# Optimization experiments

Hardware: AMD Instinct MI355X
Metric: run time of the kernel (lower is better)

## Reference

```python
import jax, jax.numpy as jnp
import numpy as np
import math

B, S, D = 2, 4096, 512
H, DK, DV = 8, 64, 64

def setup_inputs() -> dict:
    key = jax.random.key(0)
    ks = jax.random.split(key, 11)
    sc = lambda fin: 1.0 / math.sqrt(fin)
    return {
        "q": jax.random.normal(ks[0], (B, S, D), jnp.float32),
        "k": jax.random.normal(ks[1], (B, S, D), jnp.float32),
        "v": jax.random.normal(ks[2], (B, S, D), jnp.float32),
        "Wq": jax.random.normal(ks[3], (D, H * DK), jnp.float32) * sc(D),
        "bq": jnp.zeros((H * DK,), jnp.float32),
        "Wk": jax.random.normal(ks[4], (D, H * DK), jnp.float32) * sc(D),
        "bk": jnp.zeros((H * DK,), jnp.float32),
        "Wv": jax.random.normal(ks[5], (D, H * DV), jnp.float32) * sc(D),
        "bv": jnp.zeros((H * DV,), jnp.float32),
        "Wo": jax.random.normal(ks[6], (H * DV, D), jnp.float32) * sc(H * DV),
        "bo": jnp.zeros((D,), jnp.float32),
    }

def reference(q, k, v, Wq, bq, Wk, bk, Wv, bv, Wo, bo):
    b = q.shape[0]
    # projections -> [b, h, s, d]
    qh = (q @ Wq + bq).reshape(b, -1, H, DK).transpose(0, 2, 1, 3)
    kh = (k @ Wk + bk).reshape(b, -1, H, DK).transpose(0, 2, 1, 3)
    vh = (v @ Wv + bv).reshape(b, -1, H, DV).transpose(0, 2, 1, 3)
    # scores: [b, h, sq, sk]
    scores = jnp.einsum("bhqd,bhkd->bhqk", qh, kh) / math.sqrt(DK)
    # NOTE: faithful to source, softmax over dim=-2 (the QUERY axis)
    attn = jax.nn.softmax(scores, axis=-2)
    out = jnp.einsum("bhqk,bhkd->bhqd", attn, vh)
    out = out.transpose(0, 2, 1, 3).reshape(b, -1, H * DV)
    return out @ Wo + bo
```

## Files before the change

kernel.cpp:

```cpp
#include <hip/hip_runtime.h>
#include <math.h>

namespace {

typedef short bf8_t __attribute__((ext_vector_type(8)));
typedef float f32x4 __attribute__((ext_vector_type(4)));
typedef unsigned short u16;

constexpr int kB = 2, kS = 4096, kD = 512, kH = 8, kBH = 16;
constexpr float kScale = 0.125f;

__device__ __forceinline__ u16 f2bf(float x) {
  const unsigned u = __float_as_uint(x);
  return (u16)((u + 0x7FFFu + ((u >> 16) & 1u)) >> 16);
}
__device__ __forceinline__ float bf2f(u16 h) {
  return __uint_as_float(((unsigned)h) << 16);
}

template <int MODE>
__global__ __launch_bounds__(256) void gemm_kernel(
    const float* __restrict__ A, const float* __restrict__ W,
    const float* __restrict__ bias, u16* __restrict__ oHi,
    u16* __restrict__ oLo, float* __restrict__ oF) {
  __shared__ float As[16][68];
  __shared__ float Ws[16][68];
  const int t = threadIdx.x;
  const int m0 = blockIdx.y * 64;
  const int n0 = blockIdx.x * 64;
  const int ty = t >> 4, tx = t & 15;
  const int lam = t >> 2, lac = t & 3;
  const int lwk = t >> 4, lwn = t & 15;

  float acc[4][4] = {};

  for (int k0 = 0; k0 < kD; k0 += 16) {
    const float4 av = *(const float4*)&A[(size_t)(m0 + lam) * kD + k0 + lac * 4];
    const float4 wv = *(const float4*)&W[(size_t)(k0 + lwk) * kD + n0 + lwn * 4];
    __syncthreads();
    As[lac * 4 + 0][lam] = av.x;
    As[lac * 4 + 1][lam] = av.y;
    As[lac * 4 + 2][lam] = av.z;
    As[lac * 4 + 3][lam] = av.w;
    *(float4*)&Ws[lwk][lwn * 4] = wv;
    __syncthreads();
#pragma unroll
    for (int kk = 0; kk < 16; ++kk) {
      const float4 a4 = *(const float4*)&As[kk][ty * 4];
      const float4 b4 = *(const float4*)&Ws[kk][tx * 4];
      const float a[4] = {a4.x, a4.y, a4.z, a4.w};
      const float b[4] = {b4.x, b4.y, b4.z, b4.w};
#pragma unroll
      for (int i = 0; i < 4; ++i)
#pragma unroll
        for (int j = 0; j < 4; ++j) acc[i][j] = fmaf(a[i], b[j], acc[i][j]);
    }
  }

  float bb[4];
#pragma unroll
  for (int j = 0; j < 4; ++j) bb[j] = bias[n0 + tx * 4 + j];

  if (MODE == 0) {
    const int h = n0 >> 6;
#pragma unroll
    for (int i = 0; i < 4; ++i) {
      const int m = m0 + ty * 4 + i;
      const int bI = m >> 12, s = m & (kS - 1);
      const int bh = bI * kH + h;
      union { u16 u[4]; uint2 q; } ph, pl;
#pragma unroll
      for (int j = 0; j < 4; ++j) {
        const float x = acc[i][j] + bb[j];
        ph.u[j] = f2bf(x);
        pl.u[j] = f2bf(x - bf2f(ph.u[j]));
      }
      const size_t off = ((size_t)bh * kS + s) * 64 + tx * 4;
      *(uint2*)&oHi[off] = ph.q;
      *(uint2*)&oLo[off] = pl.q;
    }
  } else if (MODE == 2) {
    const int h = n0 >> 6;
    const int bI = m0 >> 12;
    const int s0 = (m0 & (kS - 1)) + ty * 4;
    const int bh = bI * kH + h;
#pragma unroll
    for (int j = 0; j < 4; ++j) {
      const int dv = tx * 4 + j;
      float4 ov;
      ov.x = acc[0][j] + bb[j];
      ov.y = acc[1][j] + bb[j];
      ov.z = acc[2][j] + bb[j];
      ov.w = acc[3][j] + bb[j];
      *(float4*)&oF[((size_t)(bh * 64 + dv)) * kS + s0] = ov;
    }
  } else {
#pragma unroll
    for (int i = 0; i < 4; ++i) {
      const int m = m0 + ty * 4 + i;
      float4 ov;
      ov.x = acc[i][0] + bb[0];
      ov.y = acc[i][1] + bb[1];
      ov.z = acc[i][2] + bb[2];
      ov.w = acc[i][3] + bb[3];
      *(float4*)&oF[(size_t)m * kD + n0 + tx * 4] = ov;
    }
  }
}

__global__ __launch_bounds__(256) void colstats_kernel(
    const u16* __restrict__ Qhi, const u16* __restrict__ Qlo,
    const u16* __restrict__ Khi, const u16* __restrict__ Klo,
    float* __restrict__ Rl) {
  const int nid = (int)blockIdx.x;
  const int swz = (nid & 7) * 128 + (nid >> 3);
  const int bh = swz >> 6;
  const int k0 = (swz & 63) << 6;
  const int t = threadIdx.x;
  const int w = t >> 6, l = t & 63;
  const int lr = l & 15, lg = l >> 4;
  const size_t base = (size_t)bh * kS * 64;

  bf8_t kbh[4][2], kbl[4][2];
#pragma unroll
  for (int nt = 0; nt < 4; ++nt)
#pragma unroll
    for (int kh = 0; kh < 2; ++kh) {
      const size_t off = base + (size_t)(k0 + nt * 16 + lr) * 64 + kh * 32 + lg * 8;
      kbh[nt][kh] = *(const bf8_t*)&Khi[off];
      kbl[nt][kh] = *(const bf8_t*)&Klo[off];
    }

  float lsum[4] = {0.f, 0.f, 0.f, 0.f};

  for (int q0 = 0; q0 < kS; q0 += 64) {
    bf8_t qah[2], qal[2];
    const size_t qoff = base + (size_t)(q0 + w * 16 + lr) * 64;
#pragma unroll
    for (int kh = 0; kh < 2; ++kh) {
      qah[kh] = *(const bf8_t*)&Qhi[qoff + kh * 32 + lg * 8];
      qal[kh] = *(const bf8_t*)&Qlo[qoff + kh * 32 + lg * 8];
    }
#pragma unroll
    for (int nt = 0; nt < 4; ++nt) {
      f32x4 acc = {0.f, 0.f, 0.f, 0.f};
#pragma unroll
      for (int kh = 0; kh < 2; ++kh) {
        acc = __builtin_amdgcn_mfma_f32_16x16x32_bf16(qah[kh], kbh[nt][kh], acc, 0, 0, 0);
        acc = __builtin_amdgcn_mfma_f32_16x16x32_bf16(qah[kh], kbl[nt][kh], acc, 0, 0, 0);
        acc = __builtin_amdgcn_mfma_f32_16x16x32_bf16(qal[kh], kbh[nt][kh], acc, 0, 0, 0);
      }
#pragma unroll
      for (int r = 0; r < 4; ++r) lsum[nt] += __expf(acc[r] * kScale);
    }
  }

#pragma unroll
  for (int nt = 0; nt < 4; ++nt) {
    float s = lsum[nt];
    s += __shfl_xor(s, 16, 64);
    s += __shfl_xor(s, 32, 64);
    lsum[nt] = s;
  }
  __shared__ float red[4][64];
  if (l < 16) {
#pragma unroll
    for (int nt = 0; nt < 4; ++nt) red[w][nt * 16 + l] = lsum[nt];
  }
  __syncthreads();
  if (t < 64) {
    const float s = red[0][t] + red[1][t] + red[2][t] + red[3][t];
    Rl[(size_t)bh * kS + k0 + t] = 1.0f / s;
  }
}

__global__ __launch_bounds__(256) void scale_split_kernel(
    const float* __restrict__ Vf, const float* __restrict__ Rl,
    u16* __restrict__ Vsh, u16* __restrict__ Vsl) {
  const int idx = blockIdx.x * 256 + threadIdx.x;
  const int s4 = (idx & 1023) << 2;
  const int bhdv = idx >> 10;
  const int bh = bhdv >> 6;
  const float4 v = *(const float4*)&Vf[(size_t)bhdv * kS + s4];
  const float4 r = *(const float4*)&Rl[(size_t)bh * kS + s4];
  const float x[4] = {v.x * r.x, v.y * r.y, v.z * r.z, v.w * r.w};
  union { u16 u[4]; uint2 q; } hh, ll;
#pragma unroll
  for (int j = 0; j < 4; ++j) {
    hh.u[j] = f2bf(x[j]);
    ll.u[j] = f2bf(x[j] - bf2f(hh.u[j]));
  }
  *(uint2*)&Vsh[(size_t)bhdv * kS + s4] = hh.q;
  *(uint2*)&Vsl[(size_t)bhdv * kS + s4] = ll.q;
}

__global__ __launch_bounds__(256) void attn_kernel(
    const u16* __restrict__ Qhi, const u16* __restrict__ Qlo,
    const u16* __restrict__ Khi, const u16* __restrict__ Klo,
    const u16* __restrict__ Vsh, const u16* __restrict__ Vsl,
    float* __restrict__ AttnOut) {
  __shared__ u16 KsH[64 * 72], KsL[64 * 72];
  __shared__ u16 VpH[64 * 72], VpL[64 * 72];

  const int nid = (int)blockIdx.x;
  const int swz = (nid & 7) * 64 + (nid >> 3);
  const int bh = swz >> 5;
  const int q0 = (swz & 31) << 7;
  const int t = threadIdx.x;
  const int w = t >> 6, l = t & 63;
  const int lr = l & 15, lg = l >> 4;
  const size_t base = (size_t)bh * kS * 64;

  const int srow = t >> 3;
  const int sc = t & 7;
  const int sc8 = sc * 8;
  const int sub = sc & 3, half = sub >> 1;
  const int posA = ((sc >> 2) << 5) + ((sub & 1) << 4) + (half << 2);

  bf8_t qh[2][2], ql[2][2];
#pragma unroll
  for (int nt = 0; nt < 2; ++nt) {
    const size_t qoff = base + (size_t)(q0 + w * 32 + nt * 16 + lr) * 64;
#pragma unroll
    for (int kh = 0; kh < 2; ++kh) {
      qh[nt][kh] = *(const bf8_t*)&Qhi[qoff + kh * 32 + lg * 8];
      ql[nt][kh] = *(const bf8_t*)&Qlo[qoff + kh * 32 + lg * 8];
    }
  }

  f32x4 acco[4][2];
  {
    const f32x4 z = {0.f, 0.f, 0.f, 0.f};
#pragma unroll
    for (int mt = 0; mt < 4; ++mt)
#pragma unroll
      for (int nt = 0; nt < 2; ++nt) acco[mt][nt] = z;
  }

  uint4 rkh[2], rkl[2], rvh[2], rvl[2];
#pragma unroll
  for (int ri = 0; ri < 2; ++ri) {
    const int row = srow + ri * 32;
    rkh[ri] = *(const uint4*)&Khi[base + (size_t)row * 64 + sc8];
    rkl[ri] = *(const uint4*)&Klo[base + (size_t)row * 64 + sc8];
    rvh[ri] = *(const uint4*)&Vsh[(size_t)(bh * 64 + row) * kS + sc8];
    rvl[ri] = *(const uint4*)&Vsl[(size_t)(bh * 64 + row) * kS + sc8];
  }

  for (int kt = 0; kt < kS / 64; ++kt) {
    __syncthreads();
#pragma unroll
    for (int ri = 0; ri < 2; ++ri) {
      const int row = srow + ri * 32;
      *(uint4*)&KsH[row * 72 + sc8] = rkh[ri];
      *(uint4*)&KsL[row * 72 + sc8] = rkl[ri];
      uint2 a, b;
      a.x = rvh[ri].x; a.y = rvh[ri].y; b.x = rvh[ri].z; b.y = rvh[ri].w;
      *(uint2*)&VpH[row * 72 + posA] = a;
      *(uint2*)&VpH[row * 72 + posA + 8] = b;
      a.x = rvl[ri].x; a.y = rvl[ri].y; b.x = rvl[ri].z; b.y = rvl[ri].w;
      *(uint2*)&VpL[row * 72 + posA] = a;
      *(uint2*)&VpL[row * 72 + posA + 8] = b;
    }
    __syncthreads();

    if (kt + 1 < kS / 64) {
      const int k0n = (kt + 1) * 64;
#pragma unroll
      for (int ri = 0; ri < 2; ++ri) {
        const int row = srow + ri * 32;
        rkh[ri] = *(const uint4*)&Khi[base + (size_t)(k0n + row) * 64 + sc8];
        rkl[ri] = *(const uint4*)&Klo[base + (size_t)(k0n + row) * 64 + sc8];
        rvh[ri] = *(const uint4*)&Vsh[(size_t)(bh * 64 + row) * kS + k0n + sc8];
        rvl[ri] = *(const uint4*)&Vsl[(size_t)(bh * 64 + row) * kS + k0n + sc8];
      }
    }

    f32x4 accs[4][2];
#pragma unroll
    for (int mt = 0; mt < 4; ++mt) {
      bf8_t kfh[2], kfl[2];
#pragma unroll
      for (int kh = 0; kh < 2; ++kh) {
        kfh[kh] = *(const bf8_t*)&KsH[(mt * 16 + lr) * 72 + kh * 32 + lg * 8];
        kfl[kh] = *(const bf8_t*)&KsL[(mt * 16 + lr) * 72 + kh * 32 + lg * 8];
      }
#pragma unroll
      for (int nt = 0; nt < 2; ++nt) {
        f32x4 a = {0.f, 0.f, 0.f, 0.f};
#pragma unroll
        for (int kh = 0; kh < 2; ++kh) {
          a = __builtin_amdgcn_mfma_f32_16x16x32_bf16(kfh[kh], qh[nt][kh], a, 0, 0, 0);
          a = __builtin_amdgcn_mfma_f32_16x16x32_bf16(kfh[kh], ql[nt][kh], a, 0, 0, 0);
          a = __builtin_amdgcn_mfma_f32_16x16x32_bf16(kfl[kh], qh[nt][kh], a, 0, 0, 0);
        }
        accs[mt][nt] = a;
      }
    }

    bf8_t ph[2][2], pl[2][2];
#pragma unroll
    for (int nt = 0; nt < 2; ++nt)
#pragma unroll
      for (int kh = 0; kh < 2; ++kh) {
        union { u16 u[8]; bf8_t v; } uh, ul;
#pragma unroll
        for (int r = 0; r < 4; ++r) {
          const float x0 = __expf(accs[2 * kh][nt][r] * kScale);
          const u16 h0 = f2bf(x0);
          uh.u[r] = h0;
          ul.u[r] = f2bf(x0 - bf2f(h0));
          const float x1 = __expf(accs[2 * kh + 1][nt][r] * kScale);
          const u16 h1 = f2bf(x1);
          uh.u[4 + r] = h1;
          ul.u[4 + r] = f2bf(x1 - bf2f(h1));
        }
        ph[nt][kh] = uh.v;
        pl[nt][kh] = ul.v;
      }

#pragma unroll
    for (int mt = 0; mt < 4; ++mt) {
      bf8_t vfh[2], vfl[2];
#pragma unroll
      for (int kh = 0; kh < 2; ++kh) {
        vfh[kh] = *(const bf8_t*)&VpH[(mt * 16 + lr) * 72 + kh * 32 + lg * 8];
        vfl[kh] = *(const bf8_t*)&VpL[(mt * 16 + lr) * 72 + kh * 32 + lg * 8];
      }
#pragma unroll
      for (int nt = 0; nt < 2; ++nt) {
        f32x4 a = acco[mt][nt];
#pragma unroll
        for (int kh = 0; kh < 2; ++kh) {
          a = __builtin_amdgcn_mfma_f32_16x16x32_bf16(vfh[kh], ph[nt][kh], a, 0, 0, 0);
          a = __builtin_amdgcn_mfma_f32_16x16x32_bf16(vfh[kh], pl[nt][kh], a, 0, 0, 0);
          a = __builtin_amdgcn_mfma_f32_16x16x32_bf16(vfl[kh], ph[nt][kh], a, 0, 0, 0);
        }
        acco[mt][nt] = a;
      }
    }
  }

  const int bI = bh >> 3, h = bh & 7;
#pragma unroll
  for (int mt = 0; mt < 4; ++mt)
#pragma unroll
    for (int nt = 0; nt < 2; ++nt) {
      const int q = q0 + w * 32 + nt * 16 + lr;
#pragma unroll
      for (int r = 0; r < 4; ++r) {
        const int dv = mt * 16 + lg * 4 + r;
        AttnOut[((size_t)(bI * kS + q)) * kD + h * 64 + dv] = acco[mt][nt][r];
      }
    }
}

}

extern "C" void kernel_launch(void* const* d_in, const int* in_sizes, int n_in,
                              void* d_out, int out_size, void* d_ws,
                              size_t ws_size, hipStream_t stream) {
  (void)in_sizes; (void)n_in; (void)out_size; (void)ws_size;
  const float* q  = (const float*)d_in[0];
  const float* k  = (const float*)d_in[1];
  const float* v  = (const float*)d_in[2];
  const float* Wq = (const float*)d_in[3];
  const float* bq = (const float*)d_in[4];
  const float* Wk = (const float*)d_in[5];
  const float* bk = (const float*)d_in[6];
  const float* Wv = (const float*)d_in[7];
  const float* bv = (const float*)d_in[8];
  const float* Wo = (const float*)d_in[9];
  const float* bo = (const float*)d_in[10];
  float* out = (float*)d_out;

  const size_t hE = (size_t)kBH * kS * 64;
  u16* Qhi = (u16*)d_ws;
  u16* Qlo = Qhi + hE;
  u16* Khi = Qlo + hE;
  u16* Klo = Khi + hE;
  u16* Vsh = Klo + hE;
  u16* Vsl = Vsh + hE;
  float* Vf = (float*)(Vsl + hE);
  float* Rl = Vf + hE;
  float* AttnOut = Vf;

  const dim3 gemmGrid(kD / 64, (kB * kS) / 64);

  gemm_kernel<0><<<gemmGrid, 256, 0, stream>>>(q, Wq, bq, Qhi, Qlo, nullptr);
  gemm_kernel<0><<<gemmGrid, 256, 0, stream>>>(k, Wk, bk, Khi, Klo, nullptr);
  gemm_kernel<2><<<gemmGrid, 256, 0, stream>>>(v, Wv, bv, nullptr, nullptr, Vf);
  colstats_kernel<<<1024, 256, 0, stream>>>(Qhi, Qlo, Khi, Klo, Rl);
  scale_split_kernel<<<4096, 256, 0, stream>>>(Vf, Rl, Vsh, Vsl);
  attn_kernel<<<512, 256, 0, stream>>>(Qhi, Qlo, Khi, Klo, Vsh, Vsl, AttnOut);
  gemm_kernel<1><<<gemmGrid, 256, 0, stream>>>(AttnOut, Wo, bo, nullptr, nullptr, out);
}
```

Measured before the change: 704.7 us.

## Move projection GEMMs to split-bf16 MFMA and swizzle LDS layouts

The FP32 FMA projection GEMMs are replaced with MFMA-based GEMMs using a hi/lo bf16 split (three MFMAs per tile), with new kernels that pre-split inputs and pre-transpose and split the weights. Other changes ride along: colstats stages Q tiles through swizzled LDS with register prefetch, attention uses XOR-swizzled LDS instead of padding, the attention output is written pre-split through an LDS transpose, and V transposition plus scaling moves into a tiled kernel. Rounding in the split now truncates the hi part instead of rounding to nearest, which could change accuracy. Extra launches and workspace traffic are added for splitting the inputs and weights.

```diff
diff --git a/kernel.cpp b/kernel.cpp
--- a/kernel.cpp
+++ b/kernel.cpp
@@ -10,100 +10,185 @@
 constexpr int kB = 2, kS = 4096, kD = 512, kH = 8, kBH = 16;
 constexpr float kScale = 0.125f;
 
-__device__ __forceinline__ u16 f2bf(float x) {
+__device__ __forceinline__ void split2(float x, u16& hi, u16& lo) {
   const unsigned u = __float_as_uint(x);
-  return (u16)((u + 0x7FFFu + ((u >> 16) & 1u)) >> 16);
-}
-__device__ __forceinline__ float bf2f(u16 h) {
-  return __uint_as_float(((unsigned)h) << 16);
+  hi = (u16)(u >> 16);
+  const float r = x - __uint_as_float(u & 0xFFFF0000u);
+  lo = (u16)(__float_as_uint(r) >> 16);
+}
+
+__global__ __launch_bounds__(256) void split_kernel(
+    const float* __restrict__ src, u16* __restrict__ dhi,
+    u16* __restrict__ dlo) {
+  const size_t i4 = ((size_t)blockIdx.x * 256 + threadIdx.x) * 4;
+  const float4 v = *(const float4*)&src[i4];
+  union { u16 u[4]; uint2 q; } h, l;
+  split2(v.x, h.u[0], l.u[0]);
+  split2(v.y, h.u[1], l.u[1]);
+  split2(v.z, h.u[2], l.u[2]);
+  split2(v.w, h.u[3], l.u[3]);
+  *(uint2*)&dhi[i4] = h.q;
+  *(uint2*)&dlo[i4] = l.q;
+}
+
+__global__ __launch_bounds__(256) void splitT_kernel(
+    const float* __restrict__ W, u16* __restrict__ whi,
+    u16* __restrict__ wlo) {
+  __shared__ float Ls[64][68];
+  const int t = threadIdx.x;
+  const int n0 = blockIdx.x * 64, k0 = blockIdx.y * 64;
+#pragma unroll
+  for (int i = 0; i < 4; ++i) {
+    const int kl = (t >> 4) + i * 16;
+    const int n4 = (t & 15) * 4;
+    const float4 v = *(const float4*)&W[(size_t)(k0 + kl) * kD + n0 + n4];
+    Ls[kl][n4 + 0] = v.x; Ls[kl][n4 + 1] = v.y;
+    Ls[kl][n4 + 2] = v.z; Ls[kl][n4 + 3] = v.w;
+  }
+  __syncthreads();
+#pragma unroll
+  for (int i = 0; i < 4; ++i) {
+    const int nl = (t >> 4) + i * 16;
+    const int k4 = (t & 15) * 4;
+    union { u16 u[4]; uint2 q; } h, l;
+#pragma unroll
+    for (int j = 0; j < 4; ++j) split2(Ls[k4 + j][nl], h.u[j], l.u[j]);
+    *(uint2*)&whi[(size_t)(n0 + nl) * kD + k0 + k4] = h.q;
+    *(uint2*)&wlo[(size_t)(n0 + nl) * kD + k0 + k4] = l.q;
+  }
 }
 
 template <int MODE>
-__global__ __launch_bounds__(256) void gemm_kernel(
-    const float* __restrict__ A, const float* __restrict__ W,
+__global__ __launch_bounds__(256) void mfma_gemm_kernel(
+    const u16* __restrict__ Ahi, const u16* __restrict__ Alo,
+    const u16* __restrict__ Whi, const u16* __restrict__ Wlo,
     const float* __restrict__ bias, u16* __restrict__ oHi,
     u16* __restrict__ oLo, float* __restrict__ oF) {
-  __shared__ float As[16][68];
-  __shared__ float Ws[16][68];
+  __shared__ u16 gsm[24576];
+  u16* AhS = gsm;
+  u16* AlS = gsm + 8192;
+  u16* WhS = gsm + 16384;
+  u16* WlS = gsm + 20480;
+
   const int t = threadIdx.x;
-  const int m0 = blockIdx.y * 64;
+  const int w = t >> 6, l = t & 63;
+  const int lr = l & 15, lg = l >> 4;
+  const int m0 = blockIdx.y * 128;
   const int n0 = blockIdx.x * 64;
-  const int ty = t >> 4, tx = t & 15;
-  const int lam = t >> 2, lac = t & 3;
-  const int lwk = t >> 4, lwn = t & 15;
-
-  float acc[4][4] = {};
-
-  for (int k0 = 0; k0 < kD; k0 += 16) {
-    const float4 av = *(const float4*)&A[(size_t)(m0 + lam) * kD + k0 + lac * 4];
-    const float4 wv = *(const float4*)&W[(size_t)(k0 + lwk) * kD + n0 + lwn * 4];
+
+  f32x4 acc[2][4];
+  {
+    const f32x4 z = {0.f, 0.f, 0.f, 0.f};
+#pragma unroll
+    for (int mt = 0; mt < 2; ++mt)
+#pragma unroll
+      for (int nt = 0; nt < 4; ++nt) acc[mt][nt] = z;
+  }
+
+  uint4 rAh[4], rAl[4], rWh[2], rWl[2];
+#pragma unroll
+  for (int i = 0; i < 4; ++i) {
+    const int p = t + i * 256, row = p >> 3, c = p & 7;
+    rAh[i] = *(const uint4*)&Ahi[(size_t)(m0 + row) * kD + c * 8];
+    rAl[i] = *(const uint4*)&Alo[(size_t)(m0 + row) * kD + c * 8];
+  }
+#pragma unroll
+  for (int i = 0; i < 2; ++i) {
+    const int p = t + i * 256, row = p >> 3, c = p & 7;
+    rWh[i] = *(const uint4*)&Whi[(size_t)(n0 + row) * kD + c * 8];
+    rWl[i] = *(const uint4*)&Wlo[(size_t)(n0 + row) * kD + c * 8];
+  }
+
+  for (int ks = 0; ks < 8; ++ks) {
     __syncthreads();
-    As[lac * 4 + 0][lam] = av.x;
-    As[lac * 4 + 1][lam] = av.y;
-    As[lac * 4 + 2][lam] = av.z;
-    As[lac * 4 + 3][lam] = av.w;
-    *(float4*)&Ws[lwk][lwn * 4] = wv;
+#pragma unroll
+    for (int i = 0; i < 4; ++i) {
+      const int p = t + i * 256, row = p >> 3, c = p & 7;
+      const int ch = (row * 8 + (c ^ (row & 7))) * 8;
+      *(uint4*)&AhS[ch] = rAh[i];
+      *(uint4*)&AlS[ch] = rAl[i];
+    }
+#pragma unroll
+    for (int i = 0; i < 2; ++i) {
+      const int p = t + i * 256, row = p >> 3, c = p & 7;
+      const int ch = (row * 8 + (c ^ (row & 7))) * 8;
+      *(uint4*)&WhS[ch] = rWh[i];
+      *(uint4*)&WlS[ch] = rWl[i];
+    }
     __syncthreads();
-#pragma unroll
-    for (int kk = 0; kk < 16; ++kk) {
-      const float4 a4 = *(const float4*)&As[kk][ty * 4];
-      const float4 b4 = *(const float4*)&Ws[kk][tx * 4];
-      const float a[4] = {a4.x, a4.y, a4.z, a4.w};
-      const float b[4] = {b4.x, b4.y, b4.z, b4.w};
-#pragma unroll
-      for (int i = 0; i < 4; ++i)
-#pragma unroll
-        for (int j = 0; j < 4; ++j) acc[i][j] = fmaf(a[i], b[j], acc[i][j]);
-    }
-  }
-
-  float bb[4];
-#pragma unroll
-  for (int j = 0; j < 4; ++j) bb[j] = bias[n0 + tx * 4 + j];
-
-  if (MODE == 0) {
-    const int h = n0 >> 6;
-#pragma unroll
-    for (int i = 0; i < 4; ++i) {
-      const int m = m0 + ty * 4 + i;
-      const int bI = m >> 12, s = m & (kS - 1);
-      const int bh = bI * kH + h;
-      union { u16 u[4]; uint2 q; } ph, pl;
-#pragma unroll
-      for (int j = 0; j < 4; ++j) {
-        const float x = acc[i][j] + bb[j];
-        ph.u[j] = f2bf(x);
-        pl.u[j] = f2bf(x - bf2f(ph.u[j]));
-      }
-      const size_t off = ((size_t)bh * kS + s) * 64 + tx * 4;
-      *(uint2*)&oHi[off] = ph.q;
-      *(uint2*)&oLo[off] = pl.q;
-    }
-  } else if (MODE == 2) {
-    const int h = n0 >> 6;
-    const int bI = m0 >> 12;
-    const int s0 = (m0 & (kS - 1)) + ty * 4;
-    const int bh = bI * kH + h;
-#pragma unroll
-    for (int j = 0; j < 4; ++j) {
-      const int dv = tx * 4 + j;
-      float4 ov;
-      ov.x = acc[0][j] + bb[j];
-      ov.y = acc[1][j] + bb[j];
-      ov.z = acc[2][j] + bb[j];
-      ov.w = acc[3][j] + bb[j];
-      *(float4*)&oF[((size_t)(bh * 64 + dv)) * kS + s0] = ov;
-    }
-  } else {
-#pragma unroll
-    for (int i = 0; i < 4; ++i) {
-      const int m = m0 + ty * 4 + i;
-      float4 ov;
-      ov.x = acc[i][0] + bb[0];
-      ov.y = acc[i][1] + bb[1];
-      ov.z = acc[i][2] + bb[2];
-      ov.w = acc[i][3] + bb[3];
-      *(float4*)&oF[(size_t)m * kD + n0 + tx * 4] = ov;
+
+    if (ks + 1 < 8) {
+      const int kk = (ks + 1) * 64;
+#pragma unroll
+      for (int i = 0; i < 4; ++i) {
+        const int p = t + i * 256, row = p >> 3, c = p & 7;
+        rAh[i] = *(const uint4*)&Ahi[(size_t)(m0 + row) * kD + kk + c * 8];
+        rAl[i] = *(const uint4*)&Alo[(size_t)(m0 + row) * kD + kk + c * 8];
+      }
+#pragma unroll
+      for (int i = 0; i < 2; ++i) {
+        const int p = t + i * 256, row = p >> 3, c = p & 7;
+        rWh[i] = *(const uint4*)&Whi[(size_t)(n0 + row) * kD + kk + c * 8];
+        rWl[i] = *(const uint4*)&Wlo[(size_t)(n0 + row) * kD + kk + c * 8];
+      }
+    }
+
+#pragma unroll
+    for (int kh = 0; kh < 2; ++kh) {
+#pragma unroll
+      for (int mt = 0; mt < 2; ++mt) {
+        const int ar = w * 32 + mt * 16 + lr;
+        const int au = (ar * 64 + ((kh * 32 + lg * 8) ^ ((ar & 7) * 8)));
+        const bf8_t ah = *(const bf8_t*)&AhS[au];
+        const bf8_t al = *(const bf8_t*)&AlS[au];
+#pragma unroll
+        for (int nt = 0; nt < 4; ++nt) {
+          const int br = nt * 16 + lr;
+          const int bu = (br * 64 + ((kh * 32 + lg * 8) ^ ((br & 7) * 8)));
+          const bf8_t bh = *(const bf8_t*)&WhS[bu];
+          const bf8_t bl = *(const bf8_t*)&WlS[bu];
+          f32x4 a = acc[mt][nt];
+          a = __builtin_amdgcn_mfma_f32_16x16x32_bf16(ah, bh, a, 0, 0, 0);
+          a = __builtin_amdgcn_mfma_f32_16x16x32_bf16(ah, bl, a, 0, 0, 0);
+          a = __builtin_amdgcn_mfma_f32_16x16x32_bf16(al, bh, a, 0, 0, 0);
+          acc[mt][nt] = a;
+        }
+      }
+    }
+  }
+
+  __syncthreads();
+  float* smf = (float*)gsm;
+#pragma unroll
+  for (int nt = 0; nt < 4; ++nt) {
+    const float bb = bias[n0 + nt * 16 + lr];
+#pragma unroll
+    for (int mt = 0; mt < 2; ++mt)
+#pragma unroll
+      for (int r = 0; r < 4; ++r)
+        smf[(w * 32 + mt * 16 + lg * 4 + r) * 64 + nt * 16 + lr] =
+            acc[mt][nt][r] + bb;
+  }
+  __syncthreads();
+#pragma unroll
+  for (int i = 0; i < 8; ++i) {
+    const int p = t + i * 256;
+    const int ml = p >> 4, n4 = (p & 15) * 4;
+    const float4 v = *(const float4*)&smf[p * 4];
+    if (MODE == 0) {
+      const int m = m0 + ml;
+      const int bh = (m >> 12) * kH + (n0 >> 6);
+      const int s = m & (kS - 1);
+      union { u16 u[4]; uint2 q; } h, lo;
+      split2(v.x, h.u[0], lo.u[0]);
+      split2(v.y, h.u[1], lo.u[1]);
+      split2(v.z, h.u[2], lo.u[2]);
+      split2(v.w, h.u[3], lo.u[3]);
+      const size_t off = ((size_t)bh * kS + s) * 64 + n4;
+      *(uint2*)&oHi[off] = h.q;
+      *(uint2*)&oLo[off] = lo.q;
+    } else {
+      *(float4*)&oF[(size_t)(m0 + ml) * kD + n0 + n4] = v;
     }
   }
 }
@@ -112,6 +197,8 @@
     const u16* __restrict__ Qhi, const u16* __restrict__ Qlo,
     const u16* __restrict__ Khi, const u16* __restrict__ Klo,
     float* __restrict__ Rl) {
+  __shared__ u16 qsm[8192];
+  __shared__ float red[4][64];
   const int nid = (int)blockIdx.x;
   const int swz = (nid & 7) * 128 + (nid >> 3);
   const int bh = swz >> 6;
@@ -126,32 +213,62 @@
   for (int nt = 0; nt < 4; ++nt)
 #pragma unroll
     for (int kh = 0; kh < 2; ++kh) {
-      const size_t off = base + (size_t)(k0 + nt * 16 + lr) * 64 + kh * 32 + lg * 8;
+      const size_t off =
+          base + (size_t)(k0 + nt * 16 + lr) * 64 + kh * 32 + lg * 8;
       kbh[nt][kh] = *(const bf8_t*)&Khi[off];
       kbl[nt][kh] = *(const bf8_t*)&Klo[off];
     }
 
   float lsum[4] = {0.f, 0.f, 0.f, 0.f};
 
-  for (int q0 = 0; q0 < kS; q0 += 64) {
+  uint4 rqh[2], rql[2];
+#pragma unroll
+  for (int i = 0; i < 2; ++i) {
+    const int p = t + i * 256, row = p >> 3, c = p & 7;
+    rqh[i] = *(const uint4*)&Qhi[base + (size_t)row * 64 + c * 8];
+    rql[i] = *(const uint4*)&Qlo[base + (size_t)row * 64 + c * 8];
+  }
+
+  for (int qt = 0; qt < kS / 64; ++qt) {
+    __syncthreads();
+#pragma unroll
+    for (int i = 0; i < 2; ++i) {
+      const int p = t + i * 256, row = p >> 3, c = p & 7;
+      const int ch = (row * 8 + (c ^ (row & 7))) * 8;
+      *(uint4*)&qsm[ch] = rqh[i];
+      *(uint4*)&qsm[4096 + ch] = rql[i];
+    }
+    __syncthreads();
+
+    if (qt + 1 < kS / 64) {
+      const size_t q0n = (size_t)(qt + 1) * 64;
+#pragma unroll
+      for (int i = 0; i < 2; ++i) {
+        const int p = t + i * 256, row = p >> 3, c = p & 7;
+        rqh[i] = *(const uint4*)&Qhi[base + (q0n + row) * 64 + c * 8];
+        rql[i] = *(const uint4*)&Qlo[base + (q0n + row) * 64 + c * 8];
+      }
+    }
+
     bf8_t qah[2], qal[2];
-    const size_t qoff = base + (size_t)(q0 + w * 16 + lr) * 64;
 #pragma unroll
     for (int kh = 0; kh < 2; ++kh) {
-      qah[kh] = *(const bf8_t*)&Qhi[qoff + kh * 32 + lg * 8];
-      qal[kh] = *(const bf8_t*)&Qlo[qoff + kh * 32 + lg * 8];
+      const int ar = w * 16 + lr;
+      const int au = ar * 64 + ((kh * 32 + lg * 8) ^ ((ar & 7) * 8));
+      qah[kh] = *(const bf8_t*)&qsm[au];
+      qal[kh] = *(const bf8_t*)&qsm[4096 + au];
     }
 #pragma unroll
     for (int nt = 0; nt < 4; ++nt) {
-      f32x4 acc = {0.f, 0.f, 0.f, 0.f};
+      f32x4 a = {0.f, 0.f, 0.f, 0.f};
 #pragma unroll
       for (int kh = 0; kh < 2; ++kh) {
-        acc = __builtin_amdgcn_mfma_f32_16x16x32_bf16(qah[kh], kbh[nt][kh], acc, 0, 0, 0);
-        acc = __builtin_amdgcn_mfma_f32_16x16x32_bf16(qah[kh], kbl[nt][kh], acc, 0, 0, 0);
-        acc = __builtin_amdgcn_mfma_f32_16x16x32_bf16(qal[kh], kbh[nt][kh], acc, 0, 0, 0);
-      }
-#pragma unroll
-      for (int r = 0; r < 4; ++r) lsum[nt] += __expf(acc[r] * kScale);
+        a = __builtin_amdgcn_mfma_f32_16x16x32_bf16(qah[kh], kbh[nt][kh], a, 0, 0, 0);
+        a = __builtin_amdgcn_mfma_f32_16x16x32_bf16(qah[kh], kbl[nt][kh], a, 0, 0, 0);
+        a = __builtin_amdgcn_mfma_f32_16x16x32_bf16(qal[kh], kbh[nt][kh], a, 0, 0, 0);
+      }
+#pragma unroll
+      for (int r = 0; r < 4; ++r) lsum[nt] += __expf(a[r] * kScale);
     }
   }
 
@@ -162,7 +279,6 @@
     s += __shfl_xor(s, 32, 64);
     lsum[nt] = s;
   }
-  __shared__ float red[4][64];
   if (l < 16) {
 #pragma unroll
     for (int nt = 0; nt < 4; ++nt) red[w][nt * 16 + l] = lsum[nt];
@@ -174,33 +290,50 @@
   }
 }
 
-__global__ __launch_bounds__(256) void scale_split_kernel(
-    const float* __restrict__ Vf, const float* __restrict__ Rl,
+__global__ __launch_bounds__(256) void vtrans_kernel(
+    const float* __restrict__ Vrm, const float* __restrict__ Rl,
     u16* __restrict__ Vsh, u16* __restrict__ Vsl) {
-  const int idx = blockIdx.x * 256 + threadIdx.x;
-  const int s4 = (idx & 1023) << 2;
-  const int bhdv = idx >> 10;
-  const int bh = bhdv >> 6;
-  const float4 v = *(const float4*)&Vf[(size_t)bhdv * kS + s4];
-  const float4 r = *(const float4*)&Rl[(size_t)bh * kS + s4];
-  const float x[4] = {v.x * r.x, v.y * r.y, v.z * r.z, v.w * r.w};
-  union { u16 u[4]; uint2 q; } hh, ll;
-#pragma unroll
-  for (int j = 0; j < 4; ++j) {
-    hh.u[j] = f2bf(x[j]);
-    ll.u[j] = f2bf(x[j] - bf2f(hh.u[j]));
-  }
-  *(uint2*)&Vsh[(size_t)bhdv * kS + s4] = hh.q;
-  *(uint2*)&Vsl[(size_t)bhdv * kS + s4] = ll.q;
+  __shared__ float Ls[64][68];
+  __shared__ float rl[64];
+  const int t = threadIdx.x;
+  const int s0 = blockIdx.x * 64;
+  const int bh = blockIdx.y;
+  const int bI = bh >> 3, h = bh & 7;
+#pragma unroll
+  for (int i = 0; i < 4; ++i) {
+    const int sl = (t >> 4) + i * 16;
+    const int d4 = (t & 15) * 4;
+    const float4 v =
+        *(const float4*)&Vrm[(size_t)(bI * kS + s0 + sl) * kD + h * 64 + d4];
+    Ls[sl][d4 + 0] = v.x; Ls[sl][d4 + 1] = v.y;
+    Ls[sl][d4 + 2] = v.z; Ls[sl][d4 + 3] = v.w;
+  }
+  if (t < 64) rl[t] = Rl[(size_t)bh * kS + s0 + t];
+  __syncthreads();
+#pragma unroll
+  for (int i = 0; i < 4; ++i) {
+    const int d = (t >> 4) + i * 16;
+    const int s4 = (t & 15) * 4;
+    union { u16 u[4]; uint2 q; } h4, l4;
+#pragma unroll
+    for (int j = 0; j < 4; ++j)
+      split2(Ls[s4 + j][d] * rl[s4 + j], h4.u[j], l4.u[j]);
+    const size_t off = (size_t)(bh * 64 + d) * kS + s0 + s4;
+    *(uint2*)&Vsh[off] = h4.q;
+    *(uint2*)&Vsl[off] = l4.q;
+  }
 }
 
 __global__ __launch_bounds__(256) void attn_kernel(
     const u16* __restrict__ Qhi, const u16* __restrict__ Qlo,
     const u16* __restrict__ Khi, const u16* __restrict__ Klo,
     const u16* __restrict__ Vsh, const u16* __restrict__ Vsl,
-    float* __restrict__ AttnOut) {
-  __shared__ u16 KsH[64 * 72], KsL[64 * 72];
-  __shared__ u16 VpH[64 * 72], VpL[64 * 72];
+    u16* __restrict__ AoHi, u16* __restrict__ AoLo) {
+  __shared__ u16 smem[16384];
+  u16* KsH = smem;
+  u16* KsL = smem + 4096;
+  u16* VpH = smem + 8192;
+  u16* VpL = smem + 12288;
 
   const int nid = (int)blockIdx.x;
   const int swz = (nid & 7) * 64 + (nid >> 3);
@@ -214,8 +347,8 @@
   const int srow = t >> 3;
   const int sc = t & 7;
   const int sc8 = sc * 8;
-  const int sub = sc & 3, half = sub >> 1;
-  const int posA = ((sc >> 2) << 5) + ((sub & 1) << 4) + (half << 2);
+  const int sub = sc & 3;
+  const int posA = ((sc >> 2) << 5) + ((sub & 1) << 4) + ((sub >> 1) << 2);
 
   bf8_t qh[2][2], ql[2][2];
 #pragma unroll
@@ -252,15 +385,16 @@
 #pragma unroll
     for (int ri = 0; ri < 2; ++ri) {
       const int row = srow + ri * 32;
-      *(uint4*)&KsH[row * 72 + sc8] = rkh[ri];
-      *(uint4*)&KsL[row * 72 + sc8] = rkl[ri];
+      const int xs = (row & 7) * 8;
+      *(uint4*)&KsH[(row * 64 + sc8) ^ xs] = rkh[ri];
+      *(uint4*)&KsL[(row * 64 + sc8) ^ xs] = rkl[ri];
       uint2 a, b;
       a.x = rvh[ri].x; a.y = rvh[ri].y; b.x = rvh[ri].z; b.y = rvh[ri].w;
-      *(uint2*)&VpH[row * 72 + posA] = a;
-      *(uint2*)&VpH[row * 72 + posA + 8] = b;
+      *(uint2*)&VpH[(row * 64 + posA) ^ xs] = a;
+      *(uint2*)&VpH[(row * 64 + posA + 8) ^ xs] = b;
       a.x = rvl[ri].x; a.y = rvl[ri].y; b.x = rvl[ri].z; b.y = rvl[ri].w;
-      *(uint2*)&VpL[row * 72 + posA] = a;
-      *(uint2*)&VpL[row * 72 + posA + 8] = b;
+      *(uint2*)&VpL[(row * 64 + posA) ^ xs] = a;
+      *(uint2*)&VpL[(row * 64 + posA + 8) ^ xs] = b;
     }
     __syncthreads();
 
@@ -282,8 +416,10 @@
       bf8_t kfh[2], kfl[2];
 #pragma unroll
       for (int kh = 0; kh < 2; ++kh) {
-        kfh[kh] = *(const bf8_t*)&KsH[(mt * 16 + lr) * 72 + kh * 32 + lg * 8];
-        kfl[kh] = *(const bf8_t*)&KsL[(mt * 16 + lr) * 72 + kh * 32 + lg * 8];
+        const int ar = mt * 16 + lr;
+        const int au = (ar * 64 + kh * 32 + lg * 8) ^ ((ar & 7) * 8);
+        kfh[kh] = *(const bf8_t*)&KsH[au];
+        kfl[kh] = *(const bf8_t*)&KsL[au];
       }
 #pragma unroll
       for (int nt = 0; nt < 2; ++nt) {
@@ -307,13 +443,9 @@
 #pragma unroll
         for (int r = 0; r < 4; ++r) {
           const float x0 = __expf(accs[2 * kh][nt][r] * kScale);
-          const u16 h0 = f2bf(x0);
-          uh.u[r] = h0;
-          ul.u[r] = f2bf(x0 - bf2f(h0));
+          split2(x0, uh.u[r], ul.u[r]);
           const float x1 = __expf(accs[2 * kh + 1][nt][r] * kScale);
-          const u16 h1 = f2bf(x1);
-          uh.u[4 + r] = h1;
-          ul.u[4 + r] = f2bf(x1 - bf2f(h1));
+          split2(x1, uh.u[4 + r], ul.u[4 + r]);
         }
         ph[nt][kh] = uh.v;
         pl[nt][kh] = ul.v;
@@ -324,8 +456,10 @@
       bf8_t vfh[2], vfl[2];
 #pragma unroll
       for (int kh = 0; kh < 2; ++kh) {
-        vfh[kh] = *(const bf8_t*)&VpH[(mt * 16 + lr) * 72 + kh * 32 + lg * 8];
-        vfl[kh] = *(const bf8_t*)&VpL[(mt * 16 + lr) * 72 + kh * 32 + lg * 8];
+        const int ar = mt * 16 + lr;
+        const int au = (ar * 64 + kh * 32 + lg * 8) ^ ((ar & 7) * 8);
+        vfh[kh] = *(const bf8_t*)&VpH[au];
+        vfl[kh] = *(const bf8_t*)&VpL[au];
       }
 #pragma unroll
       for (int nt = 0; nt < 2; ++nt) {
@@ -341,18 +475,33 @@
     }
   }
 
+  __syncthreads();
+  float* smf = (float*)smem;
+#pragma unroll
+  for (int mt = 0; mt < 4; ++mt)
+#pragma unroll
+    for (int nt = 0; nt < 2; ++nt) {
+      const int qv = w * 32 + nt * 16 + lr;
+#pragma unroll
+      for (int r = 0; r < 4; ++r)
+        smf[qv * 64 + mt * 16 + lg * 4 + r] = acco[mt][nt][r];
+    }
+  __syncthreads();
   const int bI = bh >> 3, h = bh & 7;
 #pragma unroll
-  for (int mt = 0; mt < 4; ++mt)
-#pragma unroll
-    for (int nt = 0; nt < 2; ++nt) {
-      const int q = q0 + w * 32 + nt * 16 + lr;
-#pragma unroll
-      for (int r = 0; r < 4; ++r) {
-        const int dv = mt * 16 + lg * 4 + r;
-        AttnOut[((size_t)(bI * kS + q)) * kD + h * 64 + dv] = acco[mt][nt][r];
-      }
-    }
+  for (int i = 0; i < 8; ++i) {
+    const int p = t + i * 256;
+    const int qv = p >> 4, n4 = (p & 15) * 4;
+    const float4 v = *(const float4*)&smf[p * 4];
+    union { u16 u[4]; uint2 q; } h4, l4;
+    split2(v.x, h4.u[0], l4.u[0]);
+    split2(v.y, h4.u[1], l4.u[1]);
+    split2(v.z, h4.u[2], l4.u[2]);
+    split2(v.w, h4.u[3], l4.u[3]);
+    const size_t off = (size_t)(bI * kS + q0 + qv) * kD + h * 64 + n4;
+    *(uint2*)&AoHi[off] = h4.q;
+    *(uint2*)&AoLo[off] = l4.q;
+  }
 }
 
 }
@@ -375,23 +524,44 @@
   float* out = (float*)d_out;
 
   const size_t hE = (size_t)kBH * kS * 64;
-  u16* Qhi = (u16*)d_ws;
-  u16* Qlo = Qhi + hE;
-  u16* Khi = Qlo + hE;
-  u16* Klo = Khi + hE;
-  u16* Vsh = Klo + hE;
-  u16* Vsl = Vsh + hE;
-  float* Vf = (float*)(Vsl + hE);
-  float* Rl = Vf + hE;
-  float* AttnOut = Vf;
-
-  const dim3 gemmGrid(kD / 64, (kB * kS) / 64);
-
-  gemm_kernel<0><<<gemmGrid, 256, 0, stream>>>(q, Wq, bq, Qhi, Qlo, nullptr);
-  gemm_kernel<0><<<gemmGrid, 256, 0, stream>>>(k, Wk, bk, Khi, Klo, nullptr);
-  gemm_kernel<2><<<gemmGrid, 256, 0, stream>>>(v, Wv, bv, nullptr, nullptr, Vf);
-  colstats_kernel<<<1024, 256, 0, stream>>>(Qhi, Qlo, Khi, Klo, Rl);
-  scale_split_kernel<<<4096, 256, 0, stream>>>(Vf, Rl, Vsh, Vsl);
-  attn_kernel<<<512, 256, 0, stream>>>(Qhi, Qlo, Khi, Klo, Vsh, Vsl, AttnOut);
-  gemm_kernel<1><<<gemmGrid, 256, 0, stream>>>(AttnOut, Wo, bo, nullptr, nullptr, out);
-}
+  const size_t wE = (size_t)kD * kD;
+  u16* ws = (u16*)d_ws;
+  u16* R0 = ws;
+  u16* R1 = R0 + hE;
+  u16* R2 = R1 + hE;
+  u16* R3 = R2 + hE;
+  u16* R4 = R3 + hE;
+  u16* R5 = R4 + hE;
+  u16* R6 = R5 + hE;
+  u16* R7 = R6 + hE;
+  u16* wtqH = R7 + hE;     u16* wtqL = wtqH + wE;
+  u16* wtkH = wtqL + wE;   u16* wtkL = wtkH + wE;
+  u16* wtvH = wtkL + wE;   u16* wtvL = wtvH + wE;
+  u16* wtoH = wtvL + wE;   u16* wtoL = wtoH + wE;
+  float* Rl = (float*)(wtoL + wE);
+
+  float* Vrm = (float*)R6;
+
+  const dim3 gGrid(kD / 64, (kB * kS) / 128);
+  const dim3 tGrid(8, 8);
+
+  splitT_kernel<<<tGrid, 256, 0, stream>>>(Wq, wtqH, wtqL);
+  splitT_kernel<<<tGrid, 256, 0, stream>>>(Wk, wtkH, wtkL);
+  splitT_kernel<<<tGrid, 256, 0, stream>>>(Wv, wtvH, wtvL);
+  splitT_kernel<<<tGrid, 256, 0, stream>>>(Wo, wtoH, wtoL);
+
+  split_kernel<<<4096, 256, 0, stream>>>(q, R0, R1);
+  mfma_gemm_kernel<0><<<gGrid, 256, 0, stream>>>(R0, R1, wtqH, wtqL, bq,
+                                                 R2, R3, nullptr);
+  split_kernel<<<4096, 256, 0, stream>>>(k, R0, R1);
+  mfma_gemm_kernel<0><<<gGrid, 256, 0, stream>>>(R0, R1, wtkH, wtkL, bk,
+                                                 R4, R5, nullptr);
+  split_kernel<<<4096, 256, 0, stream>>>(v, R0, R1);
+  mfma_gemm_kernel<1><<<gGrid, 256, 0, stream>>>(R0, R1, wtvH, wtvL, bv,
+                                                 nullptr, nullptr, Vrm);
+  colstats_kernel<<<1024, 256, 0, stream>>>(R2, R3, R4, R5, Rl);
+  vtrans_kernel<<<dim3(64, 16), 256, 0, stream>>>(Vrm, Rl, R0, R1);
+  attn_kernel<<<512, 256, 0, stream>>>(R2, R3, R4, R5, R0, R1, R6, R7);
+  mfma_gemm_kernel<1><<<gGrid, 256, 0, stream>>>(R6, R7, wtoH, wtoL, bo,
+                                                 nullptr, nullptr, out);
+}
```

New measurement: 1.026 ms. 45.6% more time.
